# Kernel tuning notes

Measured on AMD Instinct MI355X. Metric: run time of the kernel, lower is better.

The kernel has to match this reference:

```python
import jax, jax.numpy as jnp
import numpy as np
from jax import lax

VOCAB, EMB, HID, TAGS = 8000, 300, 512, 24  # hidden_dim=512 -> 256 per direction
B, S = 128, 512
H2 = HID // 2


def setup_inputs() -> dict:
    key = jax.random.key(0)
    ks = jax.random.split(key, 16)
    sc = 0.05
    inp = {
        "chars": jax.random.randint(ks[0], (B, S), 0, VOCAB),
        "tags": jax.random.randint(ks[1], (B, S), 0, TAGS),
        "mask": jnp.ones((B, S), dtype=bool),
        "emb": jax.random.normal(ks[2], (VOCAB, EMB), jnp.float32) * sc,
        # PyTorch LSTM layout: gates stacked [i, f, g, o]
        "w_ih_f": jax.random.normal(ks[3], (4 * H2, EMB), jnp.float32) * sc,
        "w_hh_f": jax.random.normal(ks[4], (4 * H2, H2), jnp.float32) * sc,
        "b_f": jax.random.normal(ks[5], (4 * H2,), jnp.float32) * sc,  # b_ih + b_hh fused
        "w_ih_b": jax.random.normal(ks[6], (4 * H2, EMB), jnp.float32) * sc,
        "w_hh_b": jax.random.normal(ks[7], (4 * H2, H2), jnp.float32) * sc,
        "b_b": jax.random.normal(ks[8], (4 * H2,), jnp.float32) * sc,
        "w_out": jax.random.normal(ks[9], (TAGS, HID), jnp.float32) * sc,
        "b_out": jax.random.normal(ks[10], (TAGS,), jnp.float32) * sc,
        "trans": jax.random.normal(ks[11], (TAGS, TAGS), jnp.float32) * sc,
        "start_trans": jax.random.normal(ks[12], (TAGS,), jnp.float32) * sc,
        "end_trans": jax.random.normal(ks[13], (TAGS,), jnp.float32) * sc,
    }
    return inp


def _lstm_dir(x, w_ih, w_hh, b, reverse):
    # x: [B, S, E] -> h: [B, S, H2]
    gx = jnp.einsum('bse,ge->bsg', x, w_ih) + b  # [B, S, 4*H2]

    def step(carry, g_t):
        h, c = carry
        g = g_t + h @ w_hh.T
        i, f, gg, o = jnp.split(g, 4, axis=-1)
        c = jax.nn.sigmoid(f) * c + jax.nn.sigmoid(i) * jnp.tanh(gg)
        h = jax.nn.sigmoid(o) * jnp.tanh(c)
        return (h, c), h

    init = (jnp.zeros((x.shape[0], H2), x.dtype), jnp.zeros((x.shape[0], H2), x.dtype))
    _, hs = lax.scan(step, init, jnp.swapaxes(gx, 0, 1), reverse=reverse)
    return jnp.swapaxes(hs, 0, 1)


def _crf_loss(emissions, tags, mask, trans, start_trans, end_trans):
    # torchcrf log-likelihood, reduction='mean'; loss = -mean
    b, s, t = emissions.shape
    maskf = mask.astype(emissions.dtype)
    # numerator: score of gold path
    em_t = jnp.take_along_axis(emissions, tags[..., None], axis=2)[..., 0]  # [B,S]
    tr_t = trans[tags[:, :-1], tags[:, 1:]]  # [B,S-1]
    score = start_trans[tags[:, 0]] + em_t[:, 0]
    score = score + jnp.sum((em_t[:, 1:] + tr_t) * maskf[:, 1:], axis=1)
    seq_ends = jnp.sum(mask.astype(jnp.int32), axis=1) - 1  # [B]
    last_tags = jnp.take_along_axis(tags, seq_ends[:, None], axis=1)[:, 0]
    score = score + end_trans[last_tags]
    # denominator: forward algorithm via scan
    alpha0 = start_trans + emissions[:, 0]  # [B,T]

    def step(alpha, inputs):
        em, m = inputs  # em [B,T], m [B]
        nxt = jax.nn.logsumexp(alpha[:, :, None] + trans[None] + em[:, None, :], axis=1)
        alpha = jnp.where(m[:, None], nxt, alpha)
        return alpha, None

    alpha, _ = lax.scan(step, alpha0,
                        (jnp.swapaxes(emissions[:, 1:], 0, 1), jnp.swapaxes(mask[:, 1:], 0, 1)))
    log_z = jax.nn.logsumexp(alpha + end_trans, axis=1)  # [B]
    llh = score - log_z
    return -jnp.mean(llh)


def reference(chars, tags, mask, emb, w_ih_f, w_hh_f, b_f, w_ih_b, w_hh_b, b_b,
              w_out, b_out, trans, start_trans, end_trans):
    x = emb[chars]  # [B,S,E]
    h_f = _lstm_dir(x, w_ih_f, w_hh_f, b_f, reverse=False)
    h_b = _lstm_dir(x, w_ih_b, w_hh_b, b_b, reverse=True)
    lstm_out = jnp.concatenate([h_f, h_b], axis=-1)  # [B,S,HID]
    emissions = jnp.einsum('bsh,th->bst', lstm_out, w_out) + b_out  # [B,S,TAGS]
    return _crf_loss(emissions, tags, mask, trans, start_trans, end_trans)
```

## Files before the change

### kernel.cpp

```cpp
#include <hip/hip_runtime.h>
#include <math.h>

#define BB   128
#define SS   512
#define EMBD 300
#define VOC  8000
#define NTAG 24
#define BSD  (BB*SS)

#define SW   400.0f
#define SH   512.0f
#define INVQ (1.0f / (400.0f * 512.0f))

typedef unsigned int   u32;
typedef unsigned short u16;

__device__ __forceinline__ int idot4(u32 a, u32 b, int c) {
#if __has_builtin(__builtin_amdgcn_sdot4)
    return __builtin_amdgcn_sdot4((int)a, (int)b, c, false);
#else
    int s = c;
    #pragma unroll
    for (int e = 0; e < 4; ++e) {
        int xa = ((int)(a << (24 - 8 * e))) >> 24;
        int xb = ((int)(b << (24 - 8 * e))) >> 24;
        s += xa * xb;
    }
    return s;
#endif
}
__device__ __forceinline__ u32 rdlane(u32 v, int l) {
#if __has_builtin(__builtin_amdgcn_readlane)
    return (u32)__builtin_amdgcn_readlane((int)v, l);
#else
    return (u32)__shfl((int)v, l);
#endif
}
__device__ __forceinline__ float sigm(float x) { return 1.0f / (1.0f + __expf(-x)); }
__device__ __forceinline__ float tanh_fast(float x) {
    return 1.0f - 2.0f / (__expf(2.0f * x) + 1.0f);
}
__device__ __forceinline__ int qclamp(float x, float s) {
    int v = (int)rintf(x * s);
    return v > 127 ? 127 : (v < -127 ? -127 : v);
}
__device__ __forceinline__ u32 q4(const float* p, float s) {
    u32 r = 0;
    #pragma unroll
    for (int e = 0; e < 4; ++e)
        r |= ((u32)(qclamp(p[e], s) & 0xFF)) << (8 * e);
    return r;
}

__global__ __launch_bounds__(512)
void k_packW(const float* __restrict__ w_hh_f, const float* __restrict__ w_hh_b,
             const float* __restrict__ w_out,
             u32* __restrict__ wreg, uint4* __restrict__ wlds,
             uint4* __restrict__ wstr, u32* __restrict__ woq)
{
    const int dir = blockIdx.x;
    const int t   = threadIdx.x;
    const float* w = dir ? w_hh_b : w_hh_f;
    const float* rowA = w + (size_t)t * 256;
    const float* rowB = w + (size_t)(t + 512) * 256;

    for (int q = 0; q < 16; ++q) {
        wreg[((size_t)(dir * 32 + q) * 512) + t]      = q4(rowA + 4 * q, SW);
        wreg[((size_t)(dir * 32 + 16 + q) * 512) + t] = q4(rowB + 4 * q, SW);
    }
    for (int qq = 0; qq < 7; ++qq) {
        uint4 va, vb;
        va.x = q4(rowA + 4 * (16 + 4 * qq + 0), SW);
        va.y = q4(rowA + 4 * (16 + 4 * qq + 1), SW);
        va.z = q4(rowA + 4 * (16 + 4 * qq + 2), SW);
        va.w = q4(rowA + 4 * (16 + 4 * qq + 3), SW);
        vb.x = q4(rowB + 4 * (16 + 4 * qq + 0), SW);
        vb.y = q4(rowB + 4 * (16 + 4 * qq + 1), SW);
        vb.z = q4(rowB + 4 * (16 + 4 * qq + 2), SW);
        vb.w = q4(rowB + 4 * (16 + 4 * qq + 3), SW);
        wlds[((size_t)(dir * 14 + qq) * 512) + t]     = va;
        wlds[((size_t)(dir * 14 + 7 + qq) * 512) + t] = vb;
    }
    for (int qq = 0; qq < 5; ++qq) {
        uint4 va, vb;
        va.x = q4(rowA + 4 * (44 + 4 * qq + 0), SW);
        va.y = q4(rowA + 4 * (44 + 4 * qq + 1), SW);
        va.z = q4(rowA + 4 * (44 + 4 * qq + 2), SW);
        va.w = q4(rowA + 4 * (44 + 4 * qq + 3), SW);
        vb.x = q4(rowB + 4 * (44 + 4 * qq + 0), SW);
        vb.y = q4(rowB + 4 * (44 + 4 * qq + 1), SW);
        vb.z = q4(rowB + 4 * (44 + 4 * qq + 2), SW);
        vb.w = q4(rowB + 4 * (44 + 4 * qq + 3), SW);
        wstr[((size_t)(dir * 10 + qq) * 512) + t]     = va;
        wstr[((size_t)(dir * 10 + 5 + qq) * 512) + t] = vb;
    }
    for (int i = t; i < NTAG * 64; i += 512) {
        const int tag = i >> 6, q = i & 63;
        woq[(size_t)dir * NTAG * 64 + i] =
            q4(w_out + (size_t)tag * 512 + dir * 256 + 4 * q, SW);
    }
}

__global__ __launch_bounds__(256)
void k_gxtab(const float* __restrict__ emb,
             const float* __restrict__ w_f, const float* __restrict__ bias_f,
             const float* __restrict__ w_b, const float* __restrict__ bias_b,
             u16* __restrict__ gxtab)
{
    const int dir = blockIdx.z;
    const float* W    = dir ? w_b    : w_f;
    const float* bias = dir ? bias_b : bias_f;
    u16* out = gxtab + (size_t)dir * VOC * 1024;
    const int r0 = blockIdx.y * 64;
    const int c0 = blockIdx.x * 128;

    __shared__ float As[16][65];
    __shared__ float Bs[16][129];

    const int tid = threadIdx.x;
    const int kk = tid & 15;
    const int rr = tid >> 4;
    const int ty = tid >> 4;
    const int tx = tid & 15;

    float acc[4][8] = {};

    for (int kt = 0; kt < EMBD; kt += 16) {
        const int k = kt + kk;
        const bool kok = (k < EMBD);
        #pragma unroll
        for (int p = 0; p < 4; ++p)
            As[kk][rr + p * 16] = kok ? emb[(size_t)(r0 + rr + p * 16) * EMBD + k] : 0.0f;
        #pragma unroll
        for (int p = 0; p < 8; ++p)
            Bs[kk][rr + p * 16] = kok ? W[(size_t)(c0 + rr + p * 16) * EMBD + k] : 0.0f;
        __syncthreads();
        #pragma unroll
        for (int q = 0; q < 16; ++q) {
            float av[4], bv[8];
            #pragma unroll
            for (int i = 0; i < 4; ++i) av[i] = As[q][ty * 4 + i];
            #pragma unroll
            for (int jj = 0; jj < 8; ++jj) bv[jj] = Bs[q][jj * 16 + tx];
            #pragma unroll
            for (int i = 0; i < 4; ++i)
                #pragma unroll
                for (int jj = 0; jj < 8; ++jj)
                    acc[i][jj] = fmaf(av[i], bv[jj], acc[i][jj]);
        }
        __syncthreads();
    }

    #pragma unroll
    for (int i = 0; i < 4; ++i) {
        const size_t rb = (size_t)(r0 + ty * 4 + i) * 1024;
        #pragma unroll
        for (int jj = 0; jj < 8; ++jj) {
            const int cl = c0 + jj * 16 + tx;
            out[rb + cl] = __builtin_bit_cast(u16, (_Float16)(acc[i][jj] + bias[cl]));
        }
    }
}

__global__ __launch_bounds__(512, 2)
void k_lstm_rl(const int* __restrict__ chars, const u16* __restrict__ gxtab,
               const u32* __restrict__ wreg, const uint4* __restrict__ wlds,
               const uint4* __restrict__ wstr, const u32* __restrict__ woq,
               const float* __restrict__ b_out,
               float* __restrict__ emis_f, float* __restrict__ emis_b)
{
    const int bid = blockIdx.x;
    const int dir = bid >> 7;
    const int b   = bid & 127;
    const int tid = threadIdx.x;

    __shared__ __align__(16) uint4 ldsW[14 * 512];
    __shared__ __align__(16) u32   hq[2][64];
    __shared__ __align__(16) u32   woL[NTAG * 64];
    __shared__ __align__(16) float2 xg[256];
    __shared__ int chlds[SS];

    chlds[tid] = chars[(size_t)b * SS + tid];
    {
        const uint4* wl = wlds + (size_t)dir * 14 * 512;
        #pragma unroll
        for (int q = 0; q < 14; ++q) ldsW[q * 512 + tid] = wl[(size_t)q * 512 + tid];
        const u32* wop = woq + (size_t)dir * NTAG * 64;
        for (int i = tid; i < NTAG * 64; i += 512) woL[i] = wop[i];
    }

    u32 WR[32];
    {
        const u32* wrp = wreg + (size_t)dir * 32 * 512 + tid;
        #pragma unroll
        for (int q = 0; q < 32; ++q) WR[q] = wrp[(size_t)q * 512];
    }
    const uint4* wsp = wstr + (size_t)dir * 10 * 512 + tid;

    const u16* gxp = gxtab + (size_t)dir * VOC * 1024;
    float* emis = (dir ? emis_b : emis_f) + (size_t)b * SS * NTAG;

    const int etid  = tid - 256;
    const bool edo  = (tid >= 256) && (etid < 192);
    const int etag  = etid >> 3, epart = etid & 7;
    const float bo  = (edo && dir == 0) ? b_out[etag] : 0.0f;

    float c = 0.0f;
    u32 hreg = 0u;
    __syncthreads();

    const int t0 = dir ? (SS - 1) : 0;
    u16 gA = gxp[(size_t)chlds[t0] * 1024 + tid];
    u16 gB = gxp[(size_t)chlds[t0] * 1024 + 512 + tid];

    int cur = 0;
    #pragma unroll 1
    for (int sloc = 0; sloc < SS; ++sloc) {
        const int t = dir ? (SS - 1 - sloc) : sloc;

        u16 gA_n = 0, gB_n = 0;
        if (sloc < SS - 1) {
            const int tn = dir ? (t - 1) : (t + 1);
            const size_t o = (size_t)chlds[tn] * 1024 + tid;
            gA_n = gxp[o];
            gB_n = gxp[o + 512];
        }
        uint4 s[10];
        #pragma unroll
        for (int qq = 0; qq < 10; ++qq) s[qq] = wsp[(size_t)qq * 512];

        int aA = 0, aB = 0;
        #pragma unroll
        for (int q = 0; q < 16; ++q) {
            const u32 hs = rdlane(hreg, q);
            aA = idot4(WR[q], hs, aA);
            aB = idot4(WR[16 + q], hs, aB);
        }
        #pragma unroll
        for (int qq = 0; qq < 7; ++qq) {
            const uint4 wa = ldsW[qq * 512 + tid];
            const uint4 wb = ldsW[(7 + qq) * 512 + tid];
            const u32 h0 = rdlane(hreg, 16 + 4 * qq + 0);
            const u32 h1 = rdlane(hreg, 16 + 4 * qq + 1);
            const u32 h2 = rdlane(hreg, 16 + 4 * qq + 2);
            const u32 h3 = rdlane(hreg, 16 + 4 * qq + 3);
            aA = idot4(wa.x, h0, aA); aB = idot4(wb.x, h0, aB);
            aA = idot4(wa.y, h1, aA); aB = idot4(wb.y, h1, aB);
            aA = idot4(wa.z, h2, aA); aB = idot4(wb.z, h2, aB);
            aA = idot4(wa.w, h3, aA); aB = idot4(wb.w, h3, aB);
        }
        #pragma unroll
        for (int qq = 0; qq < 5; ++qq) {
            const uint4 wa = s[qq];
            const uint4 wb = s[5 + qq];
            const u32 h0 = rdlane(hreg, 44 + 4 * qq + 0);
            const u32 h1 = rdlane(hreg, 44 + 4 * qq + 1);
            const u32 h2 = rdlane(hreg, 44 + 4 * qq + 2);
            const u32 h3 = rdlane(hreg, 44 + 4 * qq + 3);
            aA = idot4(wa.x, h0, aA); aB = idot4(wb.x, h0, aB);
            aA = idot4(wa.y, h1, aA); aB = idot4(wb.y, h1, aB);
            aA = idot4(wa.z, h2, aA); aB = idot4(wb.z, h2, aB);
            aA = idot4(wa.w, h3, aA); aB = idot4(wb.w, h3, aB);
        }
        const float apreA = (float)aA * INVQ + (float)__builtin_bit_cast(_Float16, gA);
        const float apreB = (float)aB * INVQ + (float)__builtin_bit_cast(_Float16, gB);

        if (tid >= 256) xg[tid - 256] = make_float2(sigm(apreA), sigm(apreB));
        __syncthreads();

        if (tid < 256) {
            const float2 fo = xg[tid];
            const float ig = sigm(apreA);
            const float gg = tanh_fast(apreB);
            c = fmaf(fo.x, c, ig * gg);
            const float h = fo.y * tanh_fast(c);
            const int hi = qclamp(h, SH);
            const int b1 = __shfl_down(hi, 1);
            const int b2 = __shfl_down(hi, 2);
            const int b3 = __shfl_down(hi, 3);
            if ((tid & 3) == 0)
                hq[cur ^ 1][tid >> 2] = (u32)(hi & 0xFF) | ((u32)(b1 & 0xFF) << 8) |
                                        ((u32)(b2 & 0xFF) << 16) | ((u32)(b3 & 0xFF) << 24);
        }
        __syncthreads();

        hreg = hq[cur ^ 1][tid & 63];

        if (edo) {
            const uint4* hn4 = (const uint4*)hq[cur ^ 1];
            const uint4* wp  = (const uint4*)woL;
            const uint4 h0 = hn4[epart * 2], h1 = hn4[epart * 2 + 1];
            const uint4 w0 = wp[etag * 16 + epart * 2];
            const uint4 w1 = wp[etag * 16 + epart * 2 + 1];
            int ei = idot4(w0.x, h0.x, 0);
            ei = idot4(w0.y, h0.y, ei);
            ei = idot4(w0.z, h0.z, ei);
            ei = idot4(w0.w, h0.w, ei);
            ei = idot4(w1.x, h1.x, ei);
            ei = idot4(w1.y, h1.y, ei);
            ei = idot4(w1.z, h1.z, ei);
            ei = idot4(w1.w, h1.w, ei);
            float e = (float)ei * INVQ;
            e += __shfl_down(e, 4);
            e += __shfl_down(e, 2);
            e += __shfl_down(e, 1);
            if (epart == 0) emis[(size_t)t * NTAG + etag] = e + bo;
        }
        gA = gA_n; gB = gB_n;
        cur ^= 1;
    }
}

__global__ __launch_bounds__(64)
void k_crf(const float* __restrict__ emis_f, const float* __restrict__ emis_b,
           const int* __restrict__ tags,
           const float* __restrict__ trans, const float* __restrict__ start_tr,
           const float* __restrict__ end_tr, float* __restrict__ llh)
{
    const int b    = blockIdx.x;
    const int lane = threadIdx.x;
    const float* ef = emis_f + (size_t)b * SS * NTAG;
    const float* eb = emis_b + (size_t)b * SS * NTAG;
    const int*   tg = tags + (size_t)b * SS;
    const bool active = (lane < NTAG);

    float trans_reg[NTAG];
    #pragma unroll
    for (int i = 0; i < NTAG; ++i)
        trans_reg[i] = active ? trans[i * NTAG + lane] : 0.0f;

    float sc = 0.0f;
    for (int t = lane; t < SS; t += 64) {
        const int tt = tg[t];
        sc += ef[t * NTAG + tt] + eb[t * NTAG + tt];
        if (t > 0) sc += trans[tg[t - 1] * NTAG + tt];
    }
    #pragma unroll
    for (int off = 32; off > 0; off >>= 1) sc += __shfl_down(sc, off);

    float alpha = active ? (start_tr[lane] + ef[lane] + eb[lane]) : -1e30f;
    for (int t = 1; t < SS; ++t) {
        float v[NTAG];
        #pragma unroll
        for (int i = 0; i < NTAG; ++i)
            v[i] = __shfl(alpha, i) + trans_reg[i];
        float m = v[0];
        #pragma unroll
        for (int i = 1; i < NTAG; ++i) m = fmaxf(m, v[i]);
        float ssum = 0.0f;
        #pragma unroll
        for (int i = 0; i < NTAG; ++i) ssum += __expf(v[i] - m);
        const float e = active ? (ef[t * NTAG + lane] + eb[t * NTAG + lane]) : 0.0f;
        alpha = active ? (m + __logf(ssum) + e) : -1e30f;
    }

    float v = alpha + (active ? end_tr[lane] : 0.0f);
    float m = v;
    #pragma unroll
    for (int off = 32; off > 0; off >>= 1) m = fmaxf(m, __shfl_down(m, off));
    m = __shfl(m, 0);
    float e = __expf(v - m);
    #pragma unroll
    for (int off = 32; off > 0; off >>= 1) e += __shfl_down(e, off);

    if (lane == 0) {
        const float logz  = m + __logf(e);
        const float score = sc + start_tr[tg[0]] + end_tr[tg[SS - 1]];
        llh[b] = score - logz;
    }
}

__global__ __launch_bounds__(64)
void k_final(const float* __restrict__ llh, float* __restrict__ out)
{
    const int lane = threadIdx.x;
    float v = llh[lane] + llh[lane + 64];
    #pragma unroll
    for (int off = 32; off > 0; off >>= 1) v += __shfl_down(v, off);
    if (lane == 0) out[0] = -(v * (1.0f / 128.0f));
}

extern "C" void kernel_launch(void* const* d_in, const int* in_sizes, int n_in,
                              void* d_out, int out_size, void* d_ws, size_t ws_size,
                              hipStream_t stream)
{
    (void)in_sizes; (void)n_in; (void)out_size; (void)ws_size;

    const int*   chars   = (const int*)d_in[0];
    const int*   tags    = (const int*)d_in[1];
    const float* emb     = (const float*)d_in[3];
    const float* w_ih_f  = (const float*)d_in[4];
    const float* w_hh_f  = (const float*)d_in[5];
    const float* b_f     = (const float*)d_in[6];
    const float* w_ih_b  = (const float*)d_in[7];
    const float* w_hh_b  = (const float*)d_in[8];
    const float* b_b     = (const float*)d_in[9];
    const float* w_out   = (const float*)d_in[10];
    const float* b_out   = (const float*)d_in[11];
    const float* trans   = (const float*)d_in[12];
    const float* start_t = (const float*)d_in[13];
    const float* end_t   = (const float*)d_in[14];

    char* ws = (char*)d_ws;
    size_t off = 0;
    auto carve = [&](size_t bytes) -> char* {
        char* p = ws + off;
        off += (bytes + 255) & ~(size_t)255;
        return p;
    };
    u16*   gxtab  = (u16*)carve((size_t)2 * VOC * 1024 * 2);
    u32*   wreg   = (u32*)carve((size_t)2 * 32 * 512 * 4);
    uint4* wlds   = (uint4*)carve((size_t)2 * 14 * 512 * 16);
    uint4* wstr   = (uint4*)carve((size_t)2 * 10 * 512 * 16);
    u32*   woq    = (u32*)carve((size_t)2 * NTAG * 64 * 4);
    float* emis_f = (float*)carve((size_t)BSD * NTAG * 4);
    float* emis_b = (float*)carve((size_t)BSD * NTAG * 4);
    float* llh    = (float*)carve(128 * 4);

    hipLaunchKernelGGL(k_packW, dim3(2), dim3(512), 0, stream,
                       w_hh_f, w_hh_b, w_out, wreg, wlds, wstr, woq);
    hipLaunchKernelGGL(k_gxtab, dim3(8, 125, 2), dim3(256), 0, stream,
                       emb, w_ih_f, b_f, w_ih_b, b_b, gxtab);
    hipLaunchKernelGGL(k_lstm_rl, dim3(256), dim3(512), 0, stream,
                       chars, gxtab, wreg, wlds, wstr, woq, b_out, emis_f, emis_b);
    hipLaunchKernelGGL(k_crf, dim3(128), dim3(64), 0, stream,
                       emis_f, emis_b, tags, trans, start_t, end_t, llh);
    hipLaunchKernelGGL(k_final, dim3(1), dim3(64), 0, stream,
                       llh, (float*)d_out);
}
```

Baseline: 1.179 ms.

## Move emission projection out of LSTM recurrence into separate batched kernel

The LSTM recurrence no longer computes the per-step emission dot products. It stores the quantized hidden state to global memory, and a new k_emis kernel computes emissions for both directions in one batched pass, which CRF then reads from a single array. Separately, h is now written to LDS as individual bytes instead of being packed with shuffles, and the __syncthreads calls are replaced with a raw lgkmcnt wait plus s_barrier. The goal is to shorten the serial critical path per timestep, at the cost of an extra kernel and about 32MB of hidden-state traffic.

```diff
diff --git a/kernel.cpp b/kernel.cpp
--- a/kernel.cpp
+++ b/kernel.cpp
@@ -14,6 +14,7 @@
 
 typedef unsigned int   u32;
 typedef unsigned short u16;
+typedef unsigned char  u8;
 
 __device__ __forceinline__ int idot4(u32 a, u32 b, int c) {
 #if __has_builtin(__builtin_amdgcn_sdot4)
@@ -35,6 +36,10 @@
 #else
     return (u32)__shfl((int)v, l);
 #endif
+}
+__device__ __forceinline__ void bar_lds() {
+    asm volatile("s_waitcnt lgkmcnt(0)" ::: "memory");
+    __builtin_amdgcn_s_barrier();
 }
 __device__ __forceinline__ float sigm(float x) { return 1.0f / (1.0f + __expf(-x)); }
 __device__ __forceinline__ float tanh_fast(float x) {
@@ -165,9 +170,8 @@
 __global__ __launch_bounds__(512, 2)
 void k_lstm_rl(const int* __restrict__ chars, const u16* __restrict__ gxtab,
                const u32* __restrict__ wreg, const uint4* __restrict__ wlds,
-               const uint4* __restrict__ wstr, const u32* __restrict__ woq,
-               const float* __restrict__ b_out,
-               float* __restrict__ emis_f, float* __restrict__ emis_b)
+               const uint4* __restrict__ wstr,
+               u32* __restrict__ hst)
 {
     const int bid = blockIdx.x;
     const int dir = bid >> 7;
@@ -176,7 +180,6 @@
 
     __shared__ __align__(16) uint4 ldsW[14 * 512];
     __shared__ __align__(16) u32   hq[2][64];
-    __shared__ __align__(16) u32   woL[NTAG * 64];
     __shared__ __align__(16) float2 xg[256];
     __shared__ int chlds[SS];
 
@@ -185,8 +188,6 @@
         const uint4* wl = wlds + (size_t)dir * 14 * 512;
         #pragma unroll
         for (int q = 0; q < 14; ++q) ldsW[q * 512 + tid] = wl[(size_t)q * 512 + tid];
-        const u32* wop = woq + (size_t)dir * NTAG * 64;
-        for (int i = tid; i < NTAG * 64; i += 512) woL[i] = wop[i];
     }
 
     u32 WR[32];
@@ -198,12 +199,6 @@
     const uint4* wsp = wstr + (size_t)dir * 10 * 512 + tid;
 
     const u16* gxp = gxtab + (size_t)dir * VOC * 1024;
-    float* emis = (dir ? emis_b : emis_f) + (size_t)b * SS * NTAG;
-
-    const int etid  = tid - 256;
-    const bool edo  = (tid >= 256) && (etid < 192);
-    const int etag  = etid >> 3, epart = etid & 7;
-    const float bo  = (edo && dir == 0) ? b_out[etag] : 0.0f;
 
     float c = 0.0f;
     u32 hreg = 0u;
@@ -266,7 +261,7 @@
         const float apreB = (float)aB * INVQ + (float)__builtin_bit_cast(_Float16, gB);
 
         if (tid >= 256) xg[tid - 256] = make_float2(sigm(apreA), sigm(apreB));
-        __syncthreads();
+        bar_lds();
 
         if (tid < 256) {
             const float2 fo = xg[tid];
@@ -275,52 +270,72 @@
             c = fmaf(fo.x, c, ig * gg);
             const float h = fo.y * tanh_fast(c);
             const int hi = qclamp(h, SH);
-            const int b1 = __shfl_down(hi, 1);
-            const int b2 = __shfl_down(hi, 2);
-            const int b3 = __shfl_down(hi, 3);
-            if ((tid & 3) == 0)
-                hq[cur ^ 1][tid >> 2] = (u32)(hi & 0xFF) | ((u32)(b1 & 0xFF) << 8) |
-                                        ((u32)(b2 & 0xFF) << 16) | ((u32)(b3 & 0xFF) << 24);
-        }
-        __syncthreads();
+            ((u8*)hq[cur ^ 1])[tid] = (u8)(hi & 0xFF);
+        }
+        bar_lds();
 
         hreg = hq[cur ^ 1][tid & 63];
-
-        if (edo) {
-            const uint4* hn4 = (const uint4*)hq[cur ^ 1];
-            const uint4* wp  = (const uint4*)woL;
-            const uint4 h0 = hn4[epart * 2], h1 = hn4[epart * 2 + 1];
-            const uint4 w0 = wp[etag * 16 + epart * 2];
-            const uint4 w1 = wp[etag * 16 + epart * 2 + 1];
-            int ei = idot4(w0.x, h0.x, 0);
-            ei = idot4(w0.y, h0.y, ei);
-            ei = idot4(w0.z, h0.z, ei);
-            ei = idot4(w0.w, h0.w, ei);
-            ei = idot4(w1.x, h1.x, ei);
-            ei = idot4(w1.y, h1.y, ei);
-            ei = idot4(w1.z, h1.z, ei);
-            ei = idot4(w1.w, h1.w, ei);
-            float e = (float)ei * INVQ;
-            e += __shfl_down(e, 4);
-            e += __shfl_down(e, 2);
-            e += __shfl_down(e, 1);
-            if (epart == 0) emis[(size_t)t * NTAG + etag] = e + bo;
-        }
+        if (tid < 64)
+            hst[(((size_t)b * SS + t) * 2 + dir) * 64 + tid] = hreg;
+
         gA = gA_n; gB = gB_n;
         cur ^= 1;
     }
 }
 
+__global__ __launch_bounds__(256)
+void k_emis(const u32* __restrict__ hst, const u32* __restrict__ woq,
+            const float* __restrict__ b_out, float* __restrict__ emis)
+{
+    const int r0  = blockIdx.x * 32;
+    const int tid = threadIdx.x;
+
+    __shared__ __align__(16) u32 hs[32 * 132];
+    __shared__ __align__(16) u32 wo[NTAG * 132];
+
+    #pragma unroll
+    for (int p = 0; p < 16; ++p) {
+        const int idx = p * 256 + tid;
+        const int row = idx >> 7, rest = idx & 127;
+        hs[row * 132 + rest] = hst[((size_t)(r0 + row)) * 128 + rest];
+    }
+    for (int i = tid; i < NTAG * 128; i += 256) {
+        const int tag = i >> 7, q = i & 127;
+        const u32 v = (q < 64) ? woq[tag * 64 + q]
+                               : woq[NTAG * 64 + tag * 64 + (q - 64)];
+        wo[tag * 132 + q] = v;
+    }
+    __syncthreads();
+
+    #pragma unroll
+    for (int rep = 0; rep < 3; ++rep) {
+        const int out = rep * 256 + tid;
+        const int row = out / 24;
+        const int tag = out - row * 24;
+        const uint4* h4 = (const uint4*)&hs[row * 132];
+        const uint4* w4 = (const uint4*)&wo[tag * 132];
+        int e = 0;
+        #pragma unroll
+        for (int q = 0; q < 32; ++q) {
+            const uint4 hv = h4[q];
+            const uint4 wv = w4[q];
+            e = idot4(wv.x, hv.x, e);
+            e = idot4(wv.y, hv.y, e);
+            e = idot4(wv.z, hv.z, e);
+            e = idot4(wv.w, hv.w, e);
+        }
+        emis[(size_t)(r0 + row) * NTAG + tag] = (float)e * INVQ + b_out[tag];
+    }
+}
+
 __global__ __launch_bounds__(64)
-void k_crf(const float* __restrict__ emis_f, const float* __restrict__ emis_b,
-           const int* __restrict__ tags,
+void k_crf(const float* __restrict__ emis, const int* __restrict__ tags,
            const float* __restrict__ trans, const float* __restrict__ start_tr,
            const float* __restrict__ end_tr, float* __restrict__ llh)
 {
     const int b    = blockIdx.x;
     const int lane = threadIdx.x;
-    const float* ef = emis_f + (size_t)b * SS * NTAG;
-    const float* eb = emis_b + (size_t)b * SS * NTAG;
+    const float* em = emis + (size_t)b * SS * NTAG;
     const int*   tg = tags + (size_t)b * SS;
     const bool active = (lane < NTAG);
 
@@ -332,13 +347,13 @@
     float sc = 0.0f;
     for (int t = lane; t < SS; t += 64) {
         const int tt = tg[t];
-        sc += ef[t * NTAG + tt] + eb[t * NTAG + tt];
+        sc += em[t * NTAG + tt];
         if (t > 0) sc += trans[tg[t - 1] * NTAG + tt];
     }
     #pragma unroll
     for (int off = 32; off > 0; off >>= 1) sc += __shfl_down(sc, off);
 
-    float alpha = active ? (start_tr[lane] + ef[lane] + eb[lane]) : -1e30f;
+    float alpha = active ? (start_tr[lane] + em[lane]) : -1e30f;
     for (int t = 1; t < SS; ++t) {
         float v[NTAG];
         #pragma unroll
@@ -350,7 +365,7 @@
         float ssum = 0.0f;
         #pragma unroll
         for (int i = 0; i < NTAG; ++i) ssum += __expf(v[i] - m);
-        const float e = active ? (ef[t * NTAG + lane] + eb[t * NTAG + lane]) : 0.0f;
+        const float e = active ? em[t * NTAG + lane] : 0.0f;
         alpha = active ? (m + __logf(ssum) + e) : -1e30f;
     }
 
@@ -413,8 +428,8 @@
     uint4* wlds   = (uint4*)carve((size_t)2 * 14 * 512 * 16);
     uint4* wstr   = (uint4*)carve((size_t)2 * 10 * 512 * 16);
     u32*   woq    = (u32*)carve((size_t)2 * NTAG * 64 * 4);
-    float* emis_f = (float*)carve((size_t)BSD * NTAG * 4);
-    float* emis_b = (float*)carve((size_t)BSD * NTAG * 4);
+    u32*   hst    = (u32*)carve((size_t)BSD * 2 * 64 * 4);
+    float* emis   = (float*)carve((size_t)BSD * NTAG * 4);
     float* llh    = (float*)carve(128 * 4);
 
     hipLaunchKernelGGL(k_packW, dim3(2), dim3(512), 0, stream,
@@ -422,9 +437,11 @@
     hipLaunchKernelGGL(k_gxtab, dim3(8, 125, 2), dim3(256), 0, stream,
                        emb, w_ih_f, b_f, w_ih_b, b_b, gxtab);
     hipLaunchKernelGGL(k_lstm_rl, dim3(256), dim3(512), 0, stream,
-                       chars, gxtab, wreg, wlds, wstr, woq, b_out, emis_f, emis_b);
+                       chars, gxtab, wreg, wlds, wstr, hst);
+    hipLaunchKernelGGL(k_emis, dim3(BSD / 32), dim3(256), 0, stream,
+                       hst, woq, b_out, emis);
     hipLaunchKernelGGL(k_crf, dim3(128), dim3(64), 0, stream,
-                       emis_f, emis_b, tags, trans, start_t, end_t, llh);
+                       emis, tags, trans, start_t, end_t, llh);
     hipLaunchKernelGGL(k_final, dim3(1), dim3(64), 0, stream,
                        llh, (float*)d_out);
 }
```

Result: faster. 1.107 ms (-6.1%).
